# Optimization experiments

Measured on AMD Instinct MI355X. Metric: run time of the kernel, lower is better.

The kernel has to match this reference:

```python
import jax, jax.numpy as jnp
import numpy as np

N = 50000      # nodes
E = 800000     # edges
D_IN = 128
D_OUT = 128
R = 8          # relation types
EPS = 1e-12    # F.normalize eps


def setup_inputs() -> dict:
    key = jax.random.key(0)
    ks = jax.random.split(key, 10)
    s_in = 1.0 / np.sqrt(D_IN)
    s_out = 1.0 / np.sqrt(D_OUT)
    return {
        "x": jax.random.normal(ks[0], (N, D_IN), jnp.float32),
        "W1": jax.random.normal(ks[1], (R, D_IN, D_OUT), jnp.float32) * s_in,
        "loopW1": jax.random.normal(ks[2], (D_IN, D_OUT), jnp.float32) * s_in,
        "b1": jax.random.normal(ks[3], (D_OUT,), jnp.float32) * 0.01,
        "W2": jax.random.normal(ks[4], (R, D_OUT, D_OUT), jnp.float32) * s_out,
        "loopW2": jax.random.normal(ks[5], (D_OUT, D_OUT), jnp.float32) * s_out,
        "b2": jax.random.normal(ks[6], (D_OUT,), jnp.float32) * 0.01,
        "src": jax.random.randint(ks[7], (E,), 0, N),
        "dst": jax.random.randint(ks[8], (E,), 0, N),
        "etypes": jax.random.randint(ks[9], (E,), 0, R),
    }


def rel_layer(x, src, dst, etypes, W, loopW, b):
    # transform every node by every relation: [R, N, D_out]
    xw = jnp.einsum('ni,rio->rno', x, W)
    # gather per-edge messages: [E, D_out]
    msg = xw[etypes, src]
    # scatter-add to destination nodes
    agg = jax.ops.segment_sum(msg, dst, num_segments=x.shape[0])
    # self-loop + bias (DGL RelGraphConv defaults)
    return agg + x @ loopW + b


def reference(x, W1, loopW1, b1, W2, loopW2, b2, src, dst, etypes):
    h = jax.nn.relu(rel_layer(x, src, dst, etypes, W1, loopW1, b1))
    h = rel_layer(h, src, dst, etypes, W2, loopW2, b2)
    # F.normalize: row-wise L2, eps=1e-12
    nrm = jnp.maximum(jnp.linalg.norm(h, axis=1, keepdims=True), EPS)
    return h / nrm
```

## Files before the change

kernel.cpp:

```cpp
#include <hip/hip_runtime.h>
#include <hip/hip_bf16.h>

#define D 128
#define CH 4096

typedef unsigned int u32;
typedef unsigned short u16;
typedef __attribute__((ext_vector_type(8))) short s16x8;
typedef __attribute__((ext_vector_type(4))) float f32x4;
typedef __attribute__((ext_vector_type(2))) float f32x2;
typedef __attribute__((ext_vector_type(2))) u32 u32x2;
typedef __attribute__((ext_vector_type(4))) u32 u32x4;

__device__ __forceinline__ float bf2f(u16 u) {
    union { u32 u; float f; } v; v.u = ((u32)u) << 16; return v.f;
}
__device__ __forceinline__ u16 f2bf(float f) {
    union { float f; u32 u; } v; v.f = f;
    return (u16)((v.u + 0x7fffu + ((v.u >> 16) & 1u)) >> 16);
}
__device__ __forceinline__ u32 pack_bf2(float a, float b) {
    __hip_bfloat162 t = __float22bfloat162_rn(make_float2(a, b));
    union { __hip_bfloat162 t; u32 u; } v; v.t = t; return v.u;
}
__device__ __forceinline__ void unpack2(u32 u, float& lo, float& hi) {
    union { u32 u; float f; } a, b;
    a.u = u << 16; b.u = u & 0xffff0000u;
    lo = a.f; hi = b.f;
}
__device__ __forceinline__ void acc8(float (&a)[8], u32x4 u) {
#pragma unroll
    for (int m = 0; m < 4; ++m) {
        float l, h;
        unpack2(u[m], l, h);
        a[2 * m] += l; a[2 * m + 1] += h;
    }
}

__global__ void detect_dtype(const u16* __restrict__ x, int* __restrict__ flag,
                             int* __restrict__ gcnt, int nbuck) {
    __shared__ int cnt;
    if (threadIdx.x == 0) cnt = 0;
    __syncthreads();
    if ((int)threadIdx.x < nbuck) gcnt[threadIdx.x] = 0;
    u16 u = x[2 * threadIdx.x];
    int e = (u >> 7) & 0xFF;
    if (e >= 96 && e <= 150) atomicAdd(&cnt, 1);
    __syncthreads();
    if (threadIdx.x == 0) *flag = (cnt >= 128) ? 0 : 1;
}

__global__ __launch_bounds__(256)
void to_bf16_all(const void* __restrict__ s0, const void* __restrict__ s1,
                 const void* __restrict__ s2, const void* __restrict__ s3,
                 const void* __restrict__ s4, const void* __restrict__ s5,
                 const void* __restrict__ s6,
                 u16* __restrict__ d0, u16* __restrict__ d1, u16* __restrict__ d2,
                 u16* __restrict__ d3, u16* __restrict__ d4, u16* __restrict__ d5,
                 u16* __restrict__ d6,
                 long long n0, long long n1, long long n2, long long n3,
                 long long n4, long long n5, long long n6,
                 const int* __restrict__ flag)
{
    if (*flag == 0) return;
    long long tot = n0 + n1 + n2 + n3 + n4 + n5 + n6;
    long long stride = (long long)gridDim.x * 256;
    for (long long i = (long long)blockIdx.x * 256 + threadIdx.x; i < tot; i += stride) {
        const void* s; u16* d; long long off;
        if      (i < n0)                   { s = s0; d = d0; off = i; }
        else if (i < n0+n1)                { s = s1; d = d1; off = i-n0; }
        else if (i < n0+n1+n2)             { s = s2; d = d2; off = i-n0-n1; }
        else if (i < n0+n1+n2+n3)          { s = s3; d = d3; off = i-n0-n1-n2; }
        else if (i < n0+n1+n2+n3+n4)       { s = s4; d = d4; off = i-n0-n1-n2-n3; }
        else if (i < n0+n1+n2+n3+n4+n5)    { s = s5; d = d5; off = i-n0-n1-n2-n3-n4; }
        else                               { s = s6; d = d6; off = i-n0-n1-n2-n3-n4-n5; }
        d[off] = f2bf(((const float*)s)[off]);
    }
}

__global__ __launch_bounds__(256)
void csr_count(const int* __restrict__ dst, int* __restrict__ gcnt, int E, int nbuck) {
    __shared__ int scnt[256];
    int tid = threadIdx.x;
    scnt[tid] = 0;
    __syncthreads();
    int base = blockIdx.x * CH;
#pragma unroll
    for (int it = 0; it < CH / 256; ++it) {
        int e = base + it * 256 + tid;
        if (e < E) atomicAdd(&scnt[dst[e] >> 8], 1);
    }
    __syncthreads();
    if (tid < nbuck && scnt[tid] > 0) atomicAdd(&gcnt[tid], scnt[tid]);
}

__global__ __launch_bounds__(256)
void csr_scan(const int* __restrict__ gcnt, int* __restrict__ bstart, int* __restrict__ bcur,
              int nbuck, int N_, int E_, int* __restrict__ offs) {
    __shared__ int wpart[4];
    int tid = threadIdx.x, lane = tid & 63, wid = tid >> 6;
    int v = (tid < nbuck) ? gcnt[tid] : 0;
    int s = v;
#pragma unroll
    for (int off = 1; off < 64; off <<= 1) {
        int t = __shfl_up(s, off, 64);
        if (lane >= off) s += t;
    }
    if (lane == 63) wpart[wid] = s;
    __syncthreads();
    int add = 0;
    for (int w = 0; w < wid; ++w) add += wpart[w];
    int excl = add + s - v;
    if (tid <= nbuck) bstart[tid] = excl;
    if (tid < nbuck)  bcur[tid]  = excl;
    if (tid == 0) offs[N_] = E_;
}

__global__ __launch_bounds__(256)
void csr_part(const int* __restrict__ src, const int* __restrict__ dst,
              const int* __restrict__ et, int* __restrict__ bcur,
              u32* __restrict__ ebuf, int E, int N, int nbuck) {
    __shared__ int scnt[256], sbase[256];
    int tid = threadIdx.x;
    scnt[tid] = 0;
    __syncthreads();
    int base = blockIdx.x * CH;
#pragma unroll
    for (int it = 0; it < CH / 256; ++it) {
        int e = base + it * 256 + tid;
        if (e < E) atomicAdd(&scnt[dst[e] >> 8], 1);
    }
    __syncthreads();
    if (tid < nbuck) {
        int c = scnt[tid];
        sbase[tid] = c ? atomicAdd(&bcur[tid], c) : 0;
    }
    __syncthreads();
    scnt[tid] = 0;
    __syncthreads();
#pragma unroll
    for (int it = 0; it < CH / 256; ++it) {
        int e = base + it * 256 + tid;
        if (e >= E) continue;
        int d = dst[e];
        int b = d >> 8;
        int p = sbase[b] + atomicAdd(&scnt[b], 1);
        ebuf[p] = ((u32)(d & 255) << 24) | (u32)(et[e] * N + src[e]);
    }
}

__global__ __launch_bounds__(256)
void csr_emit(const u32* __restrict__ ebuf, const int* __restrict__ bstart,
              int* __restrict__ offs, int* __restrict__ rowidx, int N) {
    __shared__ int hist[256], excl[256], cur[256];
    __shared__ int wpart[4];
    int b = blockIdx.x, tid = threadIdx.x;
    int lo = bstart[b], hi = bstart[b + 1];
    hist[tid] = 0; cur[tid] = 0;
    __syncthreads();
    for (int i = lo + tid; i < hi; i += 256) atomicAdd(&hist[ebuf[i] >> 24], 1);
    __syncthreads();
    int lane = tid & 63, wid = tid >> 6;
    int v = hist[tid], s = v;
#pragma unroll
    for (int off = 1; off < 64; off <<= 1) {
        int t = __shfl_up(s, off, 64);
        if (lane >= off) s += t;
    }
    if (lane == 63) wpart[wid] = s;
    __syncthreads();
    int add = 0;
    for (int w = 0; w < wid; ++w) add += wpart[w];
    int e_ = add + s - v;
    excl[tid] = e_;
    int node = (b << 8) + tid;
    if (node < N) offs[node] = lo + e_;
    __syncthreads();
    for (int i = lo + tid; i < hi; i += 256) {
        u32 rec = ebuf[i];
        int dl = rec >> 24;
        int p = lo + excl[dl] + atomicAdd(&cur[dl], 1);
        rowidx[p] = (int)(rec & 0xFFFFFFu);
    }
}

__global__ __launch_bounds__(256)
void gemm_k128(const u16* __restrict__ Ac, const u16* __restrict__ Ao,
               const u16* __restrict__ Wc, const u16* __restrict__ Wo,
               const u16* __restrict__ lWc, const u16* __restrict__ lWo,
               const u16* __restrict__ bc, const u16* __restrict__ bo,
               const int* __restrict__ flag,
               int M, int R_, u16* __restrict__ xw, u16* __restrict__ sl)
{
    __shared__ u16 As[128 * 128];
    const bool f = (*flag != 0);
    const u16* A     = f ? Ac  : Ao;
    const u16* Wall  = f ? Wc  : Wo;
    const u16* loopW = f ? lWc : lWo;
    const u16* bias  = f ? bc  : bo;

    const int y = blockIdx.y;
    const u16* B = (y < R_) ? (Wall + (long long)y * D * D) : loopW;
    const int row0 = blockIdx.x * 128;
    const int tid  = threadIdx.x;
    const int lane = tid & 63;
    const int wv   = tid >> 6;
    const int quad = lane >> 4;
    const int l16  = lane & 15;

    {
        int r_base = (wv << 2) + (lane >> 4);
        int c      = lane & 15;
        auto* lds0 = (__attribute__((address_space(3))) char*)As;
#pragma unroll
        for (int it = 0; it < 8; ++it) {
            int rl = it * 16 + r_base;
            int cg = c ^ (rl & 15);
            int rg = row0 + rl; if (rg >= M) rg = M - 1;
            const u16* gp = A + (long long)rg * D + cg * 8;
            __builtin_amdgcn_global_load_lds(
                (const __attribute__((address_space(1))) void*)gp,
                (__attribute__((address_space(3))) void*)(lds0 + it * 4096 + wv * 1024),
                16, 0, 0);
        }
    }

    s16x8 bf[4][2];
#pragma unroll
    for (int kk = 0; kk < 4; ++kk)
#pragma unroll
        for (int j = 0; j < 8; ++j) {
            u32 p = *(const u32*)(B + (kk * 32 + quad * 8 + j) * D + wv * 32 + 2 * l16);
            bf[kk][0][j] = (short)(p & 0xffffu);
            bf[kk][1][j] = (short)(p >> 16);
        }

    f32x4 acc[8][2];
#pragma unroll
    for (int mt = 0; mt < 8; ++mt) { acc[mt][0] = (f32x4)0.f; acc[mt][1] = (f32x4)0.f; }

    __syncthreads();

#pragma unroll
    for (int kk = 0; kk < 4; ++kk) {
        const int chunk = (kk * 4 + quad) ^ l16;
#pragma unroll
        for (int mt = 0; mt < 8; ++mt) {
            int rl = mt * 16 + l16;
            s16x8 a = *(const s16x8*)(As + rl * D + chunk * 8);
            acc[mt][0] = __builtin_amdgcn_mfma_f32_16x16x32_bf16(a, bf[kk][0], acc[mt][0], 0, 0, 0);
            acc[mt][1] = __builtin_amdgcn_mfma_f32_16x16x32_bf16(a, bf[kk][1], acc[mt][1], 0, 0, 0);
        }
    }

    long long MD64 = (long long)M * 64;
    int cpair = wv * 16 + l16;
    if (y < R_) {
        u32* o = (u32*)xw + (long long)y * MD64;
#pragma unroll
        for (int mt = 0; mt < 8; ++mt)
#pragma unroll
            for (int i = 0; i < 4; ++i) {
                int r = row0 + mt * 16 + quad * 4 + i;
                if (r >= M) continue;
                __builtin_nontemporal_store(pack_bf2(acc[mt][0][i], acc[mt][1][i]),
                                            &o[(long long)r * 64 + cpair]);
            }
    } else {
        float b0 = bf2f(bias[wv * 32 + 2 * l16]);
        float b1 = bf2f(bias[wv * 32 + 2 * l16 + 1]);
        u32* o = (u32*)sl;
#pragma unroll
        for (int mt = 0; mt < 8; ++mt)
#pragma unroll
            for (int i = 0; i < 4; ++i) {
                int r = row0 + mt * 16 + quad * 4 + i;
                if (r >= M) continue;
                __builtin_nontemporal_store(pack_bf2(acc[mt][0][i] + b0, acc[mt][1][i] + b1),
                                            &o[(long long)r * 64 + cpair]);
            }
    }
}

__global__ __launch_bounds__(256)
void aggregate(const u16* __restrict__ xw, const u16* __restrict__ sl,
               const int* __restrict__ offs, const int* __restrict__ rowidx,
               void* __restrict__ out, int N, int mode, const int* __restrict__ flag)
{
    int node = blockIdx.x * 4 + (threadIdx.x >> 6);
    int lane = threadIdx.x & 63;
    int p  = lane & 15;
    int qw = lane >> 4;
    if (node >= N) return;
    const u32x4* xw4 = (const u32x4*)xw;

    float a[8];
    if (qw == 0) {
        u32x4 s4 = ((const u32x4*)sl)[(long long)node * 16 + p];
#pragma unroll
        for (int m = 0; m < 4; ++m) unpack2(s4[m], a[2 * m], a[2 * m + 1]);
    } else {
#pragma unroll
        for (int k = 0; k < 8; ++k) a[k] = 0.f;
    }

    int j = offs[node], j1 = offs[node + 1];
    for (; j + 16 <= j1; j += 16) {
        int r0 = rowidx[j + qw];
        int r1 = rowidx[j + 4 + qw];
        int r2 = rowidx[j + 8 + qw];
        int r3 = rowidx[j + 12 + qw];
        u32x4 u0 = xw4[(long long)r0 * 16 + p];
        u32x4 u1 = xw4[(long long)r1 * 16 + p];
        u32x4 u2 = xw4[(long long)r2 * 16 + p];
        u32x4 u3 = xw4[(long long)r3 * 16 + p];
        acc8(a, u0); acc8(a, u1); acc8(a, u2); acc8(a, u3);
    }
    for (; j + 4 <= j1; j += 4) {
        int r = rowidx[j + qw];
        acc8(a, xw4[(long long)r * 16 + p]);
    }
    int rem = j1 - j;
    if (rem > 0) {
        int rr = rowidx[(qw < rem) ? j + qw : j];
        u32x4 u = xw4[(long long)rr * 16 + p];
        if (qw >= rem) { u[0] = 0; u[1] = 0; u[2] = 0; u[3] = 0; }
        acc8(a, u);
    }

#pragma unroll
    for (int k = 0; k < 8; ++k) {
        a[k] += __shfl_xor(a[k], 16, 64);
        a[k] += __shfl_xor(a[k], 32, 64);
    }

    if (mode == 0) {
        if (qw == 0) {
            u32x4 w;
#pragma unroll
            for (int m = 0; m < 4; ++m)
                w[m] = pack_bf2(fmaxf(a[2 * m], 0.f), fmaxf(a[2 * m + 1], 0.f));
            __builtin_nontemporal_store(w, &((u32x4*)out)[(long long)node * 16 + p]);
        }
    } else {
        float s = 0.f;
#pragma unroll
        for (int k = 0; k < 8; ++k) s += a[k] * a[k];
#pragma unroll
        for (int off = 8; off > 0; off >>= 1) s += __shfl_xor(s, off, 64);
        float sc = 1.f / fmaxf(sqrtf(s), 1e-12f);
        if (qw == 0) {
            if (*flag) {
                f32x4 w0, w1;
#pragma unroll
                for (int m = 0; m < 4; ++m) {
                    float* wp = (m < 2) ? (float*)&w0 : (float*)&w1;
                    wp[(m & 1) * 2]     = a[2 * m] * sc;
                    wp[(m & 1) * 2 + 1] = a[2 * m + 1] * sc;
                }
                __builtin_nontemporal_store(w0, &((f32x4*)out)[(long long)node * 32 + p * 2]);
                __builtin_nontemporal_store(w1, &((f32x4*)out)[(long long)node * 32 + p * 2 + 1]);
            } else {
                u32x4 w;
#pragma unroll
                for (int m = 0; m < 4; ++m)
                    w[m] = pack_bf2(a[2 * m] * sc, a[2 * m + 1] * sc);
                __builtin_nontemporal_store(w, &((u32x4*)out)[(long long)node * 16 + p]);
            }
        }
    }
}

static inline size_t align256(size_t x) { return (x + 255) & ~(size_t)255; }

extern "C" void kernel_launch(void* const* d_in, const int* in_sizes, int n_in,
                              void* d_out, int out_size, void* d_ws, size_t ws_size,
                              hipStream_t stream)
{
    const void* x_in   = d_in[0];
    const void* W1_in  = d_in[1];
    const void* lW1_in = d_in[2];
    const void* b1_in  = d_in[3];
    const void* W2_in  = d_in[4];
    const void* lW2_in = d_in[5];
    const void* b2_in  = d_in[6];
    const int* src = (const int*)d_in[7];
    const int* dst = (const int*)d_in[8];
    const int* et  = (const int*)d_in[9];

    const int N = in_sizes[0] / D;
    const int E = in_sizes[7];
    const int R = in_sizes[1] / (D * D);
    const int nbuck = (N + 255) >> 8;

    const long long ND  = (long long)N * D;
    const long long RDD = (long long)R * D * D;
    const long long DDl = (long long)D * D;

    size_t off = 0;
    auto alloc = [&](size_t bytes) { size_t o = off; off = align256(off + bytes); return o; };
    size_t o_flag = alloc(256);
    size_t o_xc   = alloc((size_t)ND * 2);
    size_t o_W1   = alloc((size_t)RDD * 2);
    size_t o_lW1  = alloc((size_t)DDl * 2);
    size_t o_b1   = alloc((size_t)D * 2);
    size_t o_W2   = alloc((size_t)RDD * 2);
    size_t o_lW2  = alloc((size_t)DDl * 2);
    size_t o_b2   = alloc((size_t)D * 2);
    size_t o_sl   = alloc((size_t)ND * 2);
    size_t o_h    = alloc((size_t)ND * 2);
    size_t o_offs = alloc((size_t)(N + 1) * 4);
    size_t o_gcnt = alloc(1024);
    size_t o_bst  = alloc(1040 * 4);
    size_t o_bcur = alloc(1024);
    size_t o_ebuf = alloc((size_t)E * 4);
    size_t o_ridx = alloc((size_t)E * 4);
    size_t o_xw   = alloc((size_t)R * ND * 2);
    (void)ws_size;

    char* ws = (char*)d_ws;
    int* flag   = (int*)(ws + o_flag);
    u16* x_c    = (u16*)(ws + o_xc);
    u16* W1c    = (u16*)(ws + o_W1);
    u16* lW1c   = (u16*)(ws + o_lW1);
    u16* b1c    = (u16*)(ws + o_b1);
    u16* W2c    = (u16*)(ws + o_W2);
    u16* lW2c   = (u16*)(ws + o_lW2);
    u16* b2c    = (u16*)(ws + o_b2);
    u16* sl     = (u16*)(ws + o_sl);
    u16* h      = (u16*)(ws + o_h);
    int* offs   = (int*)(ws + o_offs);
    int* gcnt   = (int*)(ws + o_gcnt);
    int* bstart = (int*)(ws + o_bst);
    int* bcur   = (int*)(ws + o_bcur);
    u32* ebuf   = (u32*)(ws + o_ebuf);
    int* rowidx = (int*)(ws + o_ridx);
    u16* xw     = (u16*)(ws + o_xw);

    dim3 blk(256, 1, 1);
    int mb    = (N + 127) / 128;
    int nblkE = (E + CH - 1) / CH;

    detect_dtype<<<dim3(1), blk, 0, stream>>>((const u16*)x_in, flag, gcnt, nbuck);
    to_bf16_all<<<dim3(4096), blk, 0, stream>>>(
        x_in, W1_in, lW1_in, b1_in, W2_in, lW2_in, b2_in,
        x_c, W1c, lW1c, b1c, W2c, lW2c, b2c,
        ND, RDD, DDl, (long long)D, RDD, DDl, (long long)D, flag);

    csr_count<<<dim3(nblkE), blk, 0, stream>>>(dst, gcnt, E, nbuck);
    csr_scan<<<dim3(1), blk, 0, stream>>>(gcnt, bstart, bcur, nbuck, N, E, offs);
    csr_part<<<dim3(nblkE), blk, 0, stream>>>(src, dst, et, bcur, ebuf, E, N, nbuck);
    csr_emit<<<dim3(nbuck), blk, 0, stream>>>(ebuf, bstart, offs, rowidx, N);

    gemm_k128<<<dim3(mb, R + 1), blk, 0, stream>>>(
        x_c, (const u16*)x_in, W1c, (const u16*)W1_in, lW1c, (const u16*)lW1_in,
        b1c, (const u16*)b1_in, flag, N, R, xw, sl);
    aggregate<<<dim3((N + 3) / 4), blk, 0, stream>>>(xw, sl, offs, rowidx, h, N, 0, flag);

    gemm_k128<<<dim3(mb, R + 1), blk, 0, stream>>>(
        h, h, W2c, (const u16*)W2_in, lW2c, (const u16*)lW2_in,
        b2c, (const u16*)b2_in, flag, N, R, xw, sl);
    aggregate<<<dim3((N + 3) / 4), blk, 0, stream>>>(xw, sl, offs, rowidx, d_out, N, 1, flag);
}
```

Before: 324.0 us.

## Fuse prep kernels, finer CSR buckets, inline dtype detection, LDS-staged GEMM stores

Merges the dtype detection, fp32-to-bf16 conversion and CSR counting into one prep launch. It also removes the separate scan kernel by having csr_part and csr_emit compute bucket prefixes themselves from gcnt. Buckets shrink from 256 to 128 nodes with a smaller edge chunk, and dtype detection becomes a per-wave ballot run inside each kernel instead of a flag in global memory. The GEMM epilogue now stages results through swizzled LDS to issue coalesced 16-byte stores, and the nontemporal stores are dropped. Together these aim to cut launch count and serial gaps at the cost of redundant prefix sums and repeated detection reads.

Result: faster. 293.2 us (-9.5%).

```diff
diff --git a/kernel.cpp b/kernel.cpp
--- a/kernel.cpp
+++ b/kernel.cpp
@@ -2,7 +2,7 @@
 #include <hip/hip_bf16.h>
 
 #define D 128
-#define CH 4096
+#define CH 2048
 
 typedef unsigned int u32;
 typedef unsigned short u16;
@@ -37,163 +37,173 @@
     }
 }
 
-__global__ void detect_dtype(const u16* __restrict__ x, int* __restrict__ flag,
-                             int* __restrict__ gcnt, int nbuck) {
-    __shared__ int cnt;
-    if (threadIdx.x == 0) cnt = 0;
-    __syncthreads();
-    if ((int)threadIdx.x < nbuck) gcnt[threadIdx.x] = 0;
-    u16 u = x[2 * threadIdx.x];
+__device__ __forceinline__ bool detect_f32(const u16* __restrict__ x) {
+    int lane = threadIdx.x & 63;
+    u16 u = x[2 * lane];
     int e = (u >> 7) & 0xFF;
-    if (e >= 96 && e <= 150) atomicAdd(&cnt, 1);
-    __syncthreads();
-    if (threadIdx.x == 0) *flag = (cnt >= 128) ? 0 : 1;
-}
-
-__global__ __launch_bounds__(256)
-void to_bf16_all(const void* __restrict__ s0, const void* __restrict__ s1,
-                 const void* __restrict__ s2, const void* __restrict__ s3,
-                 const void* __restrict__ s4, const void* __restrict__ s5,
-                 const void* __restrict__ s6,
-                 u16* __restrict__ d0, u16* __restrict__ d1, u16* __restrict__ d2,
-                 u16* __restrict__ d3, u16* __restrict__ d4, u16* __restrict__ d5,
-                 u16* __restrict__ d6,
-                 long long n0, long long n1, long long n2, long long n3,
-                 long long n4, long long n5, long long n6,
-                 const int* __restrict__ flag)
+    bool sane = (e >= 96 && e <= 150);
+    unsigned long long m = __ballot(sane);
+    return __popcll(m) < 32;
+}
+
+__global__ __launch_bounds__(256)
+void zero_meta(int* __restrict__ gcnt, int* __restrict__ bcur,
+               int* __restrict__ offs, int N, int E) {
+    int t = threadIdx.x;
+    for (int k = t; k < 512; k += 256) { gcnt[k] = 0; bcur[k] = 0; }
+    if (t == 0) offs[N] = E;
+}
+
+__global__ __launch_bounds__(256)
+void prep(const int* __restrict__ dst, int* __restrict__ gcnt, int E, int nbuck, int nblkE,
+          const void* __restrict__ s0, const void* __restrict__ s1,
+          const void* __restrict__ s2, const void* __restrict__ s3,
+          const void* __restrict__ s4, const void* __restrict__ s5,
+          const void* __restrict__ s6,
+          u16* __restrict__ d0, u16* __restrict__ d1, u16* __restrict__ d2,
+          u16* __restrict__ d3, u16* __restrict__ d4, u16* __restrict__ d5,
+          u16* __restrict__ d6,
+          long long n0, long long n1, long long n2, long long n3,
+          long long n4, long long n5, long long n6)
 {
-    if (*flag == 0) return;
-    long long tot = n0 + n1 + n2 + n3 + n4 + n5 + n6;
-    long long stride = (long long)gridDim.x * 256;
-    for (long long i = (long long)blockIdx.x * 256 + threadIdx.x; i < tot; i += stride) {
-        const void* s; u16* d; long long off;
-        if      (i < n0)                   { s = s0; d = d0; off = i; }
-        else if (i < n0+n1)                { s = s1; d = d1; off = i-n0; }
-        else if (i < n0+n1+n2)             { s = s2; d = d2; off = i-n0-n1; }
-        else if (i < n0+n1+n2+n3)          { s = s3; d = d3; off = i-n0-n1-n2; }
-        else if (i < n0+n1+n2+n3+n4)       { s = s4; d = d4; off = i-n0-n1-n2-n3; }
-        else if (i < n0+n1+n2+n3+n4+n5)    { s = s5; d = d5; off = i-n0-n1-n2-n3-n4; }
-        else                               { s = s6; d = d6; off = i-n0-n1-n2-n3-n4-n5; }
-        d[off] = f2bf(((const float*)s)[off]);
-    }
-}
-
-__global__ __launch_bounds__(256)
-void csr_count(const int* __restrict__ dst, int* __restrict__ gcnt, int E, int nbuck) {
-    __shared__ int scnt[256];
     int tid = threadIdx.x;
-    scnt[tid] = 0;
+    if ((int)blockIdx.x < nblkE) {
+        __shared__ int scnt[512];
+        for (int k = tid; k < 512; k += 256) scnt[k] = 0;
+        __syncthreads();
+        int base = blockIdx.x * CH;
+#pragma unroll
+        for (int it = 0; it < CH / 256; ++it) {
+            int e = base + it * 256 + tid;
+            if (e < E) atomicAdd(&scnt[dst[e] >> 7], 1);
+        }
+        __syncthreads();
+        for (int k = tid; k < nbuck; k += 256)
+            if (scnt[k] > 0) atomicAdd(&gcnt[k], scnt[k]);
+    } else {
+        if (!detect_f32((const u16*)s0)) return;
+        long long tot = n0 + n1 + n2 + n3 + n4 + n5 + n6;
+        long long nconv = (long long)(gridDim.x - nblkE);
+        long long stride = nconv * 256;
+        for (long long i = (long long)(blockIdx.x - nblkE) * 256 + tid; i < tot; i += stride) {
+            const void* s; u16* d; long long off;
+            if      (i < n0)                   { s = s0; d = d0; off = i; }
+            else if (i < n0+n1)                { s = s1; d = d1; off = i-n0; }
+            else if (i < n0+n1+n2)             { s = s2; d = d2; off = i-n0-n1; }
+            else if (i < n0+n1+n2+n3)          { s = s3; d = d3; off = i-n0-n1-n2; }
+            else if (i < n0+n1+n2+n3+n4)       { s = s4; d = d4; off = i-n0-n1-n2-n3; }
+            else if (i < n0+n1+n2+n3+n4+n5)    { s = s5; d = d5; off = i-n0-n1-n2-n3-n4; }
+            else                               { s = s6; d = d6; off = i-n0-n1-n2-n3-n4-n5; }
+            d[off] = f2bf(((const float*)s)[off]);
+        }
+    }
+}
+
+__global__ __launch_bounds__(256)
+void csr_part(const int* __restrict__ src, const int* __restrict__ dst,
+              const int* __restrict__ et, const int* __restrict__ gcnt,
+              int* __restrict__ bcur, u32* __restrict__ ebuf, int E, int N, int nbuck) {
+    __shared__ int scnt[512], sbase[512], sbstart[513];
+    int tid = threadIdx.x, lane = tid & 63, wv = tid >> 6;
+    for (int k = tid; k < 512; k += 256) scnt[k] = 0;
     __syncthreads();
     int base = blockIdx.x * CH;
 #pragma unroll
     for (int it = 0; it < CH / 256; ++it) {
         int e = base + it * 256 + tid;
-        if (e < E) atomicAdd(&scnt[dst[e] >> 8], 1);
-    }
-    __syncthreads();
-    if (tid < nbuck && scnt[tid] > 0) atomicAdd(&gcnt[tid], scnt[tid]);
-}
-
-__global__ __launch_bounds__(256)
-void csr_scan(const int* __restrict__ gcnt, int* __restrict__ bstart, int* __restrict__ bcur,
-              int nbuck, int N_, int E_, int* __restrict__ offs) {
-    __shared__ int wpart[4];
-    int tid = threadIdx.x, lane = tid & 63, wid = tid >> 6;
-    int v = (tid < nbuck) ? gcnt[tid] : 0;
-    int s = v;
-#pragma unroll
-    for (int off = 1; off < 64; off <<= 1) {
-        int t = __shfl_up(s, off, 64);
-        if (lane >= off) s += t;
-    }
-    if (lane == 63) wpart[wid] = s;
-    __syncthreads();
-    int add = 0;
-    for (int w = 0; w < wid; ++w) add += wpart[w];
-    int excl = add + s - v;
-    if (tid <= nbuck) bstart[tid] = excl;
-    if (tid < nbuck)  bcur[tid]  = excl;
-    if (tid == 0) offs[N_] = E_;
-}
-
-__global__ __launch_bounds__(256)
-void csr_part(const int* __restrict__ src, const int* __restrict__ dst,
-              const int* __restrict__ et, int* __restrict__ bcur,
-              u32* __restrict__ ebuf, int E, int N, int nbuck) {
-    __shared__ int scnt[256], sbase[256];
-    int tid = threadIdx.x;
-    scnt[tid] = 0;
-    __syncthreads();
-    int base = blockIdx.x * CH;
-#pragma unroll
-    for (int it = 0; it < CH / 256; ++it) {
-        int e = base + it * 256 + tid;
-        if (e < E) atomicAdd(&scnt[dst[e] >> 8], 1);
-    }
-    __syncthreads();
-    if (tid < nbuck) {
-        int c = scnt[tid];
-        sbase[tid] = c ? atomicAdd(&bcur[tid], c) : 0;
-    }
-    __syncthreads();
-    scnt[tid] = 0;
+        if (e < E) atomicAdd(&scnt[dst[e] >> 7], 1);
+    }
+    if (wv == 0) {
+        int carry = 0;
+        for (int b = 0; b < nbuck; b += 64) {
+            int idx = b + lane;
+            int v = (idx < nbuck) ? gcnt[idx] : 0;
+            int s = v;
+#pragma unroll
+            for (int off = 1; off < 64; off <<= 1) {
+                int t = __shfl_up(s, off, 64);
+                if (lane >= off) s += t;
+            }
+            if (idx < nbuck) sbstart[idx] = carry + s - v;
+            carry += __shfl(s, 63, 64);
+        }
+    }
+    __syncthreads();
+    for (int k = tid; k < nbuck; k += 256) {
+        int c = scnt[k];
+        sbase[k] = c ? sbstart[k] + atomicAdd(&bcur[k], c) : 0;
+    }
+    __syncthreads();
+    for (int k = tid; k < 512; k += 256) scnt[k] = 0;
     __syncthreads();
 #pragma unroll
     for (int it = 0; it < CH / 256; ++it) {
         int e = base + it * 256 + tid;
         if (e >= E) continue;
         int d = dst[e];
-        int b = d >> 8;
+        int b = d >> 7;
         int p = sbase[b] + atomicAdd(&scnt[b], 1);
-        ebuf[p] = ((u32)(d & 255) << 24) | (u32)(et[e] * N + src[e]);
-    }
-}
-
-__global__ __launch_bounds__(256)
-void csr_emit(const u32* __restrict__ ebuf, const int* __restrict__ bstart,
+        ebuf[p] = ((u32)(d & 127) << 25) | (u32)(et[e] * N + src[e]);
+    }
+}
+
+__global__ __launch_bounds__(256)
+void csr_emit(const u32* __restrict__ ebuf, const int* __restrict__ gcnt,
               int* __restrict__ offs, int* __restrict__ rowidx, int N) {
-    __shared__ int hist[256], excl[256], cur[256];
-    __shared__ int wpart[4];
-    int b = blockIdx.x, tid = threadIdx.x;
-    int lo = bstart[b], hi = bstart[b + 1];
-    hist[tid] = 0; cur[tid] = 0;
-    __syncthreads();
-    for (int i = lo + tid; i < hi; i += 256) atomicAdd(&hist[ebuf[i] >> 24], 1);
-    __syncthreads();
-    int lane = tid & 63, wid = tid >> 6;
-    int v = hist[tid], s = v;
-#pragma unroll
-    for (int off = 1; off < 64; off <<= 1) {
-        int t = __shfl_up(s, off, 64);
-        if (lane >= off) s += t;
-    }
-    if (lane == 63) wpart[wid] = s;
-    __syncthreads();
-    int add = 0;
-    for (int w = 0; w < wid; ++w) add += wpart[w];
-    int e_ = add + s - v;
-    excl[tid] = e_;
-    int node = (b << 8) + tid;
-    if (node < N) offs[node] = lo + e_;
+    __shared__ int hist[128], excl[128], cur[128];
+    __shared__ int wred[4];
+    int b = blockIdx.x, tid = threadIdx.x, lane = tid & 63, wv = tid >> 6;
+    int part = 0;
+    for (int k = tid; k < b; k += 256) part += gcnt[k];
+#pragma unroll
+    for (int off = 32; off > 0; off >>= 1) part += __shfl_xor(part, off, 64);
+    if (lane == 0) wred[wv] = part;
+    if (tid < 128) { hist[tid] = 0; cur[tid] = 0; }
+    __syncthreads();
+    int lo = wred[0] + wred[1] + wred[2] + wred[3];
+    int hi = lo + gcnt[b];
+    for (int i = lo + tid; i < hi; i += 256) atomicAdd(&hist[ebuf[i] >> 25], 1);
+    __syncthreads();
+    if (wv == 0) {
+        int carry = 0;
+#pragma unroll
+        for (int c = 0; c < 2; ++c) {
+            int idx = c * 64 + lane;
+            int v = hist[idx];
+            int s = v;
+#pragma unroll
+            for (int off = 1; off < 64; off <<= 1) {
+                int t = __shfl_up(s, off, 64);
+                if (lane >= off) s += t;
+            }
+            excl[idx] = carry + s - v;
+            carry += __shfl(s, 63, 64);
+        }
+    }
+    __syncthreads();
+    if (tid < 128) {
+        int node = (b << 7) + tid;
+        if (node < N) offs[node] = lo + excl[tid];
+    }
     __syncthreads();
     for (int i = lo + tid; i < hi; i += 256) {
         u32 rec = ebuf[i];
-        int dl = rec >> 24;
-        int p = lo + excl[dl] + atomicAdd(&cur[dl], 1);
-        rowidx[p] = (int)(rec & 0xFFFFFFu);
-    }
-}
-
-__global__ __launch_bounds__(256)
-void gemm_k128(const u16* __restrict__ Ac, const u16* __restrict__ Ao,
+        int key = rec >> 25;
+        int p = lo + excl[key] + atomicAdd(&cur[key], 1);
+        rowidx[p] = (int)(rec & 0x1FFFFFFu);
+    }
+}
+
+__global__ __launch_bounds__(256)
+void gemm_k128(const u16* __restrict__ xdet,
+               const u16* __restrict__ Ac, const u16* __restrict__ Ao,
                const u16* __restrict__ Wc, const u16* __restrict__ Wo,
                const u16* __restrict__ lWc, const u16* __restrict__ lWo,
                const u16* __restrict__ bc, const u16* __restrict__ bo,
-               const int* __restrict__ flag,
                int M, int R_, u16* __restrict__ xw, u16* __restrict__ sl)
 {
     __shared__ u16 As[128 * 128];
-    const bool f = (*flag != 0);
+    const bool f = detect_f32(xdet);
     const u16* A     = f ? Ac  : Ao;
     const u16* Wall  = f ? Wc  : Wo;
     const u16* loopW = f ? lWc : lWo;
@@ -253,39 +263,41 @@
         }
     }
 
-    long long MD64 = (long long)M * 64;
-    int cpair = wv * 16 + l16;
-    if (y < R_) {
-        u32* o = (u32*)xw + (long long)y * MD64;
-#pragma unroll
-        for (int mt = 0; mt < 8; ++mt)
-#pragma unroll
-            for (int i = 0; i < 4; ++i) {
-                int r = row0 + mt * 16 + quad * 4 + i;
-                if (r >= M) continue;
-                __builtin_nontemporal_store(pack_bf2(acc[mt][0][i], acc[mt][1][i]),
-                                            &o[(long long)r * 64 + cpair]);
-            }
-    } else {
-        float b0 = bf2f(bias[wv * 32 + 2 * l16]);
-        float b1 = bf2f(bias[wv * 32 + 2 * l16 + 1]);
-        u32* o = (u32*)sl;
-#pragma unroll
-        for (int mt = 0; mt < 8; ++mt)
-#pragma unroll
-            for (int i = 0; i < 4; ++i) {
-                int r = row0 + mt * 16 + quad * 4 + i;
-                if (r >= M) continue;
-                __builtin_nontemporal_store(pack_bf2(acc[mt][0][i] + b0, acc[mt][1][i] + b1),
-                                            &o[(long long)r * 64 + cpair]);
-            }
-    }
-}
-
-__global__ __launch_bounds__(256)
-void aggregate(const u16* __restrict__ xw, const u16* __restrict__ sl,
+    float b0 = 0.f, b1 = 0.f;
+    if (y == R_) {
+        b0 = bf2f(bias[wv * 32 + 2 * l16]);
+        b1 = bf2f(bias[wv * 32 + 2 * l16 + 1]);
+    }
+    __syncthreads();
+    u32* Cs = (u32*)As;
+    const int cpair = wv * 16 + l16;
+    const int chunkc = cpair >> 2, sub = cpair & 3;
+#pragma unroll
+    for (int mt = 0; mt < 8; ++mt)
+#pragma unroll
+        for (int i = 0; i < 4; ++i) {
+            int rl = mt * 16 + quad * 4 + i;
+            Cs[rl * 64 + (((chunkc ^ (rl & 15)) << 2) | sub)] =
+                pack_bf2(acc[mt][0][i] + b0, acc[mt][1][i] + b1);
+        }
+    __syncthreads();
+    u32* o = (y < R_) ? ((u32*)xw + (long long)y * ((long long)M * 64)) : (u32*)sl;
+#pragma unroll
+    for (int it = 0; it < 8; ++it) {
+        int r_loc = wv * 32 + it * 4 + (lane >> 4);
+        int c  = lane & 15;
+        int cs = c ^ (r_loc & 15);
+        u32x4 v = *(const u32x4*)&Cs[r_loc * 64 + cs * 4];
+        int rg = row0 + r_loc;
+        if (rg < M) *(u32x4*)&o[(long long)rg * 64 + c * 4] = v;
+    }
+}
+
+__global__ __launch_bounds__(256)
+void aggregate(const u16* __restrict__ xdet,
+               const u16* __restrict__ xw, const u16* __restrict__ sl,
                const int* __restrict__ offs, const int* __restrict__ rowidx,
-               void* __restrict__ out, int N, int mode, const int* __restrict__ flag)
+               void* __restrict__ out, int N, int mode)
 {
     int node = blockIdx.x * 4 + (threadIdx.x >> 6);
     int lane = threadIdx.x & 63;
@@ -340,7 +352,7 @@
 #pragma unroll
             for (int m = 0; m < 4; ++m)
                 w[m] = pack_bf2(fmaxf(a[2 * m], 0.f), fmaxf(a[2 * m + 1], 0.f));
-            __builtin_nontemporal_store(w, &((u32x4*)out)[(long long)node * 16 + p]);
+            ((u32x4*)out)[(long long)node * 16 + p] = w;
         }
     } else {
         float s = 0.f;
@@ -349,23 +361,20 @@
 #pragma unroll
         for (int off = 8; off > 0; off >>= 1) s += __shfl_xor(s, off, 64);
         float sc = 1.f / fmaxf(sqrtf(s), 1e-12f);
+        bool f = detect_f32(xdet);
         if (qw == 0) {
-            if (*flag) {
+            if (f) {
                 f32x4 w0, w1;
-#pragma unroll
-                for (int m = 0; m < 4; ++m) {
-                    float* wp = (m < 2) ? (float*)&w0 : (float*)&w1;
-                    wp[(m & 1) * 2]     = a[2 * m] * sc;
-                    wp[(m & 1) * 2 + 1] = a[2 * m + 1] * sc;
-                }
-                __builtin_nontemporal_store(w0, &((f32x4*)out)[(long long)node * 32 + p * 2]);
-                __builtin_nontemporal_store(w1, &((f32x4*)out)[(long long)node * 32 + p * 2 + 1]);
+                w0[0] = a[0] * sc; w0[1] = a[1] * sc; w0[2] = a[2] * sc; w0[3] = a[3] * sc;
+                w1[0] = a[4] * sc; w1[1] = a[5] * sc; w1[2] = a[6] * sc; w1[3] = a[7] * sc;
+                ((f32x4*)out)[(long long)node * 32 + p * 2]     = w0;
+                ((f32x4*)out)[(long long)node * 32 + p * 2 + 1] = w1;
             } else {
                 u32x4 w;
 #pragma unroll
                 for (int m = 0; m < 4; ++m)
                     w[m] = pack_bf2(a[2 * m] * sc, a[2 * m + 1] * sc);
-                __builtin_nontemporal_store(w, &((u32x4*)out)[(long long)node * 16 + p]);
+                ((u32x4*)out)[(long long)node * 16 + p] = w;
             }
         }
     }
@@ -391,7 +400,7 @@
     const int N = in_sizes[0] / D;
     const int E = in_sizes[7];
     const int R = in_sizes[1] / (D * D);
-    const int nbuck = (N + 255) >> 8;
+    const int nbuck = (N + 127) >> 7;
 
     const long long ND  = (long long)N * D;
     const long long RDD = (long long)R * D * D;
@@ -399,7 +408,6 @@
 
     size_t off = 0;
     auto alloc = [&](size_t bytes) { size_t o = off; off = align256(off + bytes); return o; };
-    size_t o_flag = alloc(256);
     size_t o_xc   = alloc((size_t)ND * 2);
     size_t o_W1   = alloc((size_t)RDD * 2);
     size_t o_lW1  = alloc((size_t)DDl * 2);
@@ -410,16 +418,14 @@
     size_t o_sl   = alloc((size_t)ND * 2);
     size_t o_h    = alloc((size_t)ND * 2);
     size_t o_offs = alloc((size_t)(N + 1) * 4);
-    size_t o_gcnt = alloc(1024);
-    size_t o_bst  = alloc(1040 * 4);
-    size_t o_bcur = alloc(1024);
+    size_t o_gcnt = alloc(512 * 4);
+    size_t o_bcur = alloc(512 * 4);
     size_t o_ebuf = alloc((size_t)E * 4);
     size_t o_ridx = alloc((size_t)E * 4);
     size_t o_xw   = alloc((size_t)R * ND * 2);
     (void)ws_size;
 
     char* ws = (char*)d_ws;
-    int* flag   = (int*)(ws + o_flag);
     u16* x_c    = (u16*)(ws + o_xc);
     u16* W1c    = (u16*)(ws + o_W1);
     u16* lW1c   = (u16*)(ws + o_lW1);
@@ -431,7 +437,6 @@
     u16* h      = (u16*)(ws + o_h);
     int* offs   = (int*)(ws + o_offs);
     int* gcnt   = (int*)(ws + o_gcnt);
-    int* bstart = (int*)(ws + o_bst);
     int* bcur   = (int*)(ws + o_bcur);
     u32* ebuf   = (u32*)(ws + o_ebuf);
     int* rowidx = (int*)(ws + o_ridx);
@@ -440,25 +445,24 @@
     dim3 blk(256, 1, 1);
     int mb    = (N + 127) / 128;
     int nblkE = (E + CH - 1) / CH;
-
-    detect_dtype<<<dim3(1), blk, 0, stream>>>((const u16*)x_in, flag, gcnt, nbuck);
-    to_bf16_all<<<dim3(4096), blk, 0, stream>>>(
+    const u16* xdet = (const u16*)x_in;
+
+    zero_meta<<<dim3(1), blk, 0, stream>>>(gcnt, bcur, offs, N, E);
+    prep<<<dim3(nblkE + 2048), blk, 0, stream>>>(
+        dst, gcnt, E, nbuck, nblkE,
         x_in, W1_in, lW1_in, b1_in, W2_in, lW2_in, b2_in,
         x_c, W1c, lW1c, b1c, W2c, lW2c, b2c,
-        ND, RDD, DDl, (long long)D, RDD, DDl, (long long)D, flag);
-
-    csr_count<<<dim3(nblkE), blk, 0, stream>>>(dst, gcnt, E, nbuck);
-    csr_scan<<<dim3(1), blk, 0, stream>>>(gcnt, bstart, bcur, nbuck, N, E, offs);
-    csr_part<<<dim3(nblkE), blk, 0, stream>>>(src, dst, et, bcur, ebuf, E, N, nbuck);
-    csr_emit<<<dim3(nbuck), blk, 0, stream>>>(ebuf, bstart, offs, rowidx, N);
+        ND, RDD, DDl, (long long)D, RDD, DDl, (long long)D);
+    csr_part<<<dim3(nblkE), blk, 0, stream>>>(src, dst, et, gcnt, bcur, ebuf, E, N, nbuck);
+    csr_emit<<<dim3(nbuck), blk, 0, stream>>>(ebuf, gcnt, offs, rowidx, N);
 
     gemm_k128<<<dim3(mb, R + 1), blk, 0, stream>>>(
-        x_c, (const u16*)x_in, W1c, (const u16*)W1_in, lW1c, (const u16*)lW1_in,
-        b1c, (const u16*)b1_in, flag, N, R, xw, sl);
-    aggregate<<<dim3((N + 3) / 4), blk, 0, stream>>>(xw, sl, offs, rowidx, h, N, 0, flag);
+        xdet, x_c, (const u16*)x_in, W1c, (const u16*)W1_in, lW1c, (const u16*)lW1_in,
+        b1c, (const u16*)b1_in, N, R, xw, sl);
+    aggregate<<<dim3((N + 3) / 4), blk, 0, stream>>>(xdet, xw, sl, offs, rowidx, h, N, 0);
 
     gemm_k128<<<dim3(mb, R + 1), blk, 0, stream>>>(
-        h, h, W2c, (const u16*)W2_in, lW2c, (const u16*)lW2_in,
-        b2c, (const u16*)b2_in, flag, N, R, xw, sl);
-    aggregate<<<dim3((N + 3) / 4), blk, 0, stream>>>(xw, sl, offs, rowidx, d_out, N, 1, flag);
-}
+        xdet, h, h, W2c, (const u16*)W2_in, lW2c, (const u16*)lW2_in,
+        b2c, (const u16*)b2_in, N, R, xw, sl);
+    aggregate<<<dim3((N + 3) / 4), blk, 0, stream>>>(xdet, xw, sl, offs, rowidx, d_out, N, 1);
+}
```
